# Performance work log

Hardware: AMD Instinct MI355X
Metric: run time of the kernel (lower is better)

Reference implementation:

```python
import jax, jax.numpy as jnp
import numpy as np

B, T, D = 2048, 60, 6
H, F, O = 64, 10, 1


def setup_inputs() -> dict:
    key = jax.random.key(0)
    ks = jax.random.split(key, 16)
    w = lambda k, shape, s=0.1: jax.random.normal(k, shape, jnp.float32) * s
    return {
        "x": jax.random.normal(ks[0], (B, T, D), jnp.float32),
        "W_i": w(ks[1], (D, H)), "U_i": w(ks[2], (H, H)), "b_i": jnp.zeros((H,), jnp.float32),
        "W_ste": w(ks[3], (D, H)), "U_ste": w(ks[4], (H, H)), "b_ste": jnp.ones((H,), jnp.float32),
        "W_fre": w(ks[5], (D, F)), "U_fre": w(ks[6], (H, F)), "b_fre": jnp.ones((F,), jnp.float32),
        "W_c": w(ks[7], (D, H)), "U_c": w(ks[8], (H, H)), "b_c": jnp.zeros((H,), jnp.float32),
        "W_o": w(ks[9], (D, H)), "U_o": w(ks[10], (H, H)), "b_o": jnp.zeros((H,), jnp.float32),
        "U_a": w(ks[11], (F, 1)), "b_a": jnp.zeros((H,), jnp.float32),
        "W_p": w(ks[12], (H, O)), "b_p": jnp.zeros((O,), jnp.float32),
    }


def _hsig(v):
    # torch.nn.Hardsigmoid: relu6(x + 3) / 6
    return jnp.clip(v / 6.0 + 0.5, 0.0, 1.0)


def reference(x, W_i, U_i, b_i, W_ste, U_ste, b_ste, W_fre, U_fre, b_fre,
              W_c, U_c, b_c, W_o, U_o, b_o, U_a, b_a, W_p, b_p):
    b, t_len, _ = x.shape
    h_dim = W_i.shape[1]
    f_dim = W_fre.shape[1]
    freq = jnp.arange(f_dim, dtype=x.dtype) / f_dim  # (F,)
    ua = U_a[:, 0]  # (F,)

    def step(carry, x_t):
        h, S_re, S_im, t = carry
        i = _hsig(x_t @ W_i + b_i + h @ U_i)              # (B,H)
        ste = _hsig(x_t @ W_ste + b_ste + h @ U_ste)      # (B,H)
        fre = _hsig(x_t @ W_fre + b_fre + h @ U_fre)      # (B,F)
        f = ste[:, :, None] * fre[:, None, :]             # (B,H,F)
        c = i * jnp.tanh(x_t @ W_c + b_c + h @ U_c)       # (B,H)
        t = t + 1.0
        omega = (2.0 * jnp.pi) * t * freq                  # (F,)
        S_re = f * S_re + c[:, :, None] * jnp.cos(omega)   # (B,H,F)
        S_im = f * S_im + c[:, :, None] * jnp.sin(omega)   # (B,H,F)
        A = S_re * S_re + S_im * S_im                      # (B,H,F)
        a = jnp.tanh(jnp.einsum('bhf,f->bh', A, ua) + b_a)
        o = _hsig(x_t @ W_o + b_o + h @ U_o)
        h = o * a
        return (h, S_re, S_im, t), None

    init = (jnp.zeros((b, h_dim), x.dtype),
            jnp.zeros((b, h_dim, f_dim), x.dtype),
            jnp.zeros((b, h_dim, f_dim), x.dtype),
            jnp.asarray(0.0, x.dtype))
    (h, _, _, _), _ = jax.lax.scan(step, init, jnp.swapaxes(x, 0, 1))
    # original returns p from the last timestep only
    return h @ W_p + b_p
```

## Files before the change

### kernel.cpp

```cpp
#include <hip/hip_runtime.h>


#define BB 2048
#define TT 60
#define DD 6
#define HH 64
#define FF 10

typedef short bf16x8 __attribute__((ext_vector_type(8)));
typedef float f32x4  __attribute__((ext_vector_type(4)));

__device__ __forceinline__ unsigned short f2bf(float f) {
    union { float f; unsigned u; } v; v.f = f;
    unsigned r = v.u + 0x7fffu + ((v.u >> 16) & 1u);
    return (unsigned short)(r >> 16);
}
__device__ __forceinline__ float bf2f(unsigned short b) {
    union { unsigned u; float f; } v; v.u = ((unsigned)b) << 16; return v.f;
}

__device__ __forceinline__ float hsig_f(float v) {
    return fminf(fmaxf(fmaf(v, 0.16666666666666666f, 0.5f), 0.0f), 1.0f);
}
__device__ __forceinline__ float tanh_f(float x) {
    float xc = fminf(fmaxf(x, -12.0f), 12.0f);
    float e  = __builtin_amdgcn_exp2f(xc * 2.8853900817779268f);
    return (e - 1.0f) * __builtin_amdgcn_rcpf(e + 1.0f);
}
__device__ __forceinline__ float uni(float v) {
    return __int_as_float(__builtin_amdgcn_readfirstlane(__float_as_int(v)));
}
__device__ __forceinline__ void pinv(bf16x8& v) { asm volatile("" : "+v"(v)); }

__global__ __launch_bounds__(256)
__attribute__((amdgpu_waves_per_eu(1, 1)))
void sfm_kernel(
    const float* __restrict__ x,
    const float* __restrict__ W_i,  const float* __restrict__ U_i,  const float* __restrict__ b_i,
    const float* __restrict__ W_ste,const float* __restrict__ U_ste,const float* __restrict__ b_ste,
    const float* __restrict__ W_fre,const float* __restrict__ U_fre,const float* __restrict__ b_fre,
    const float* __restrict__ W_c,  const float* __restrict__ U_c,  const float* __restrict__ b_c,
    const float* __restrict__ W_o,  const float* __restrict__ U_o,  const float* __restrict__ b_o,
    const float* __restrict__ U_a,  const float* __restrict__ b_a,
    const float* __restrict__ W_p,  const float* __restrict__ b_p,
    float* __restrict__ out)
{
    const int tid  = threadIdx.x;
    const int lane = tid & 63;
    const int wave = tid >> 6;
    const int q    = lane >> 4;
    const int n16  = lane & 15;
    const int b0   = blockIdx.x * 8;

    __shared__ __align__(16) float xbuf[8 * TT * DD];
    __shared__ __align__(16) float hbuf[8 * 68];
    __shared__ __align__(16) float zbuf[4 * 64 * 12];
    __shared__ __align__(16) float frebuf[16 * 12];

    {
        const float4* xg = (const float4*)(x + (size_t)b0 * TT * DD);
        float4* xs = (float4*)xbuf;
        for (int i = tid; i < (8 * TT * DD) / 4; i += 256) xs[i] = xg[i];
    }
    for (int i = tid; i < 8 * 68; i += 256) hbuf[i] = 0.0f;

    const float* Ug = (wave == 0) ? U_i : (wave == 1) ? U_ste : (wave == 2) ? U_c : U_o;
    const float* Wg = (wave == 0) ? W_i : (wave == 1) ? W_ste : (wave == 2) ? W_c : W_o;
    const float* bg = (wave == 0) ? b_i : (wave == 1) ? b_ste : (wave == 2) ? b_c : b_o;

    bf16x8 Bh[5][3], Bl[5][3];
    #pragma unroll
    for (int t = 0; t < 5; ++t) {
        #pragma unroll
        for (int c = 0; c < 3; ++c) {
            #pragma unroll
            for (int j = 0; j < 8; ++j) {
                const int kv = c * 32 + q * 8 + j;
                float v = 0.0f;
                if (t < 4) {
                    const int n = t * 16 + n16;
                    if      (kv < 64) v = Ug[kv * HH + n];
                    else if (kv < 70) v = Wg[(kv - 64) * HH + n];
                    else if (kv == 70) v = bg[n];
                } else if (wave == 3 && n16 < FF) {
                    if      (kv < 64) v = U_fre[kv * FF + n16];
                    else if (kv < 70) v = W_fre[(kv - 64) * FF + n16];
                    else if (kv == 70) v = b_fre[n16];
                }
                const unsigned short hb = f2bf(v);
                const float lo = v - bf2f(hb);
                Bh[t][c][j] = (short)hb;
                Bl[t][c][j] = (short)f2bf(lo);
            }
            pinv(Bh[t][c]); pinv(Bl[t][c]);
        }
    }

    const int pb = tid >> 5;
    const int pp = tid & 31;
    const float ba0 = b_a[pp], ba1 = b_a[pp + 32];
    const float wp0 = W_p[pp], wp1 = W_p[pp + 32];
    const float bpv = uni(b_p[0]);
    float uav[FF];
    #pragma unroll
    for (int f = 0; f < FF; ++f) uav[f] = uni(U_a[f]);

    const float CBt[FF] = { 1.0f,  0.8090169943749475f,  0.30901699437494745f,
                           -0.30901699437494745f, -0.8090169943749475f, -1.0f,
                           -0.8090169943749475f, -0.30901699437494745f,
                            0.30901699437494745f,  0.8090169943749475f };
    const float SBt[FF] = { 0.0f,  0.5877852522924731f,  0.9510565162951535f,
                            0.9510565162951535f,  0.5877852522924731f,  0.0f,
                           -0.5877852522924731f, -0.9510565162951535f,
                           -0.9510565162951535f, -0.5877852522924731f };

    float Sre0[FF], Sim0[FF], Sre1[FF], Sim1[FF], cs[FF], sn[FF];
    #pragma unroll
    for (int f = 0; f < FF; ++f) {
        Sre0[f] = 0.0f; Sim0[f] = 0.0f; Sre1[f] = 0.0f; Sim1[f] = 0.0f;
        cs[f] = CBt[f]; sn[f] = SBt[f];
    }
    float h0v = 0.0f, h1v = 0.0f;

    __syncthreads();

    int sm = 0;
    for (int s = 0; s < TT; ++s) {
        bf16x8 Ah[3], Al[3];
        {
            const int ab = n16 & 7;
            #pragma unroll
            for (int c = 0; c < 2; ++c) {
                const float* hp = &hbuf[ab * 68 + c * 32 + q * 8];
                const float4 v0 = *(const float4*)hp;
                const float4 v1 = *(const float4*)(hp + 4);
                const float tv[8] = {v0.x, v0.y, v0.z, v0.w, v1.x, v1.y, v1.z, v1.w};
                #pragma unroll
                for (int j = 0; j < 8; ++j) {
                    const unsigned short hb = f2bf(tv[j]);
                    const float lo = tv[j] - bf2f(hb);
                    Ah[c][j] = (short)hb; Al[c][j] = (short)f2bf(lo);
                }
            }
            float tv[8] = {0, 0, 0, 0, 0, 0, 0, 0};
            if (q == 0) {
                const float2* x2 = (const float2*)&xbuf[ab * (TT * DD) + s * DD];
                const float2 a = x2[0], b = x2[1], c2 = x2[2];
                tv[0] = a.x; tv[1] = a.y; tv[2] = b.x; tv[3] = b.y; tv[4] = c2.x; tv[5] = c2.y;
                tv[6] = 1.0f;
            }
            #pragma unroll
            for (int j = 0; j < 8; ++j) {
                const unsigned short hb = f2bf(tv[j]);
                const float lo = tv[j] - bf2f(hb);
                Ah[2][j] = (short)hb; Al[2][j] = (short)f2bf(lo);
            }
        }

        f32x4 acc[5];
        #pragma unroll
        for (int t = 0; t < 5; ++t) {
            if (t < 4 || wave == 3) {
                f32x4 a = {0.0f, 0.0f, 0.0f, 0.0f};
                #pragma unroll
                for (int c = 0; c < 3; ++c) {
                    a = __builtin_amdgcn_mfma_f32_16x16x32_bf16(Al[c], Bh[t][c], a, 0, 0, 0);
                    a = __builtin_amdgcn_mfma_f32_16x16x32_bf16(Ah[c], Bl[t][c], a, 0, 0, 0);
                    a = __builtin_amdgcn_mfma_f32_16x16x32_bf16(Ah[c], Bh[t][c], a, 0, 0, 0);
                }
                acc[t] = a;
            }
        }

        if (lane < 32) {
            #pragma unroll
            for (int t = 0; t < 4; ++t)
                *(f32x4*)&zbuf[(wave * 64 + t * 16 + n16) * 12 + q * 4] = acc[t];
            if (wave == 3 && n16 < FF)
                *(f32x4*)&frebuf[n16 * 12 + q * 4] = acc[4];
        }
        __syncthreads();

        const float zi0 = zbuf[(0 * 64 + pp) * 12 + pb], zi1 = zbuf[(0 * 64 + pp + 32) * 12 + pb];
        const float zs0 = zbuf[(1 * 64 + pp) * 12 + pb], zs1 = zbuf[(1 * 64 + pp + 32) * 12 + pb];
        const float zc0 = zbuf[(2 * 64 + pp) * 12 + pb], zc1 = zbuf[(2 * 64 + pp + 32) * 12 + pb];
        const float zo0 = zbuf[(3 * 64 + pp) * 12 + pb], zo1 = zbuf[(3 * 64 + pp + 32) * 12 + pb];
        float fr[FF];
        #pragma unroll
        for (int f = 0; f < FF; ++f) fr[f] = hsig_f(frebuf[f * 12 + pb]);

        const float i0 = hsig_f(zi0), st0 = hsig_f(zs0), o0 = hsig_f(zo0);
        const float i1 = hsig_f(zi1), st1 = hsig_f(zs1), o1 = hsig_f(zo1);
        const float c0 = i0 * tanh_f(zc0);
        const float c1 = i1 * tanh_f(zc1);

        if (sm == 0) {
            #pragma unroll
            for (int f = 0; f < FF; ++f) { cs[f] = CBt[f]; sn[f] = SBt[f]; }
        }

        float a0 = ba0, a1 = ba1;
        #pragma unroll
        for (int f = 0; f < FF; ++f) {
            const float fc0 = st0 * fr[f], fc1 = st1 * fr[f];
            Sre0[f] = fmaf(fc0, Sre0[f], c0 * cs[f]);
            Sim0[f] = fmaf(fc0, Sim0[f], c0 * sn[f]);
            Sre1[f] = fmaf(fc1, Sre1[f], c1 * cs[f]);
            Sim1[f] = fmaf(fc1, Sim1[f], c1 * sn[f]);
            const float A0 = fmaf(Sim0[f], Sim0[f], Sre0[f] * Sre0[f]);
            const float A1 = fmaf(Sim1[f], Sim1[f], Sre1[f] * Sre1[f]);
            a0 = fmaf(A0, uav[f], a0);
            a1 = fmaf(A1, uav[f], a1);
            const float cc = cs[f];
            cs[f] = fmaf(cc, CBt[f], -(sn[f] * SBt[f]));
            sn[f] = fmaf(cc, SBt[f],   sn[f] * CBt[f]);
        }
        h0v = o0 * tanh_f(a0);
        h1v = o1 * tanh_f(a1);
        hbuf[pb * 68 + pp]      = h0v;
        hbuf[pb * 68 + pp + 32] = h1v;
        if (++sm == 10) sm = 0;
        __syncthreads();
    }

    float val = fmaf(h0v, wp0, h1v * wp1);
    #pragma unroll
    for (int off = 16; off > 0; off >>= 1) val += __shfl_xor(val, off, 64);
    if (pp == 0) out[b0 + pb] = val + bpv;
}

extern "C" void kernel_launch(void* const* d_in, const int* in_sizes, int n_in,
                              void* d_out, int out_size, void* d_ws, size_t ws_size,
                              hipStream_t stream) {
    (void)in_sizes; (void)n_in; (void)d_ws; (void)ws_size; (void)out_size;
    const float* x     = (const float*)d_in[0];
    const float* W_i   = (const float*)d_in[1];
    const float* U_i   = (const float*)d_in[2];
    const float* b_i   = (const float*)d_in[3];
    const float* W_ste = (const float*)d_in[4];
    const float* U_ste = (const float*)d_in[5];
    const float* b_ste = (const float*)d_in[6];
    const float* W_fre = (const float*)d_in[7];
    const float* U_fre = (const float*)d_in[8];
    const float* b_fre = (const float*)d_in[9];
    const float* W_c   = (const float*)d_in[10];
    const float* U_c   = (const float*)d_in[11];
    const float* b_c   = (const float*)d_in[12];
    const float* W_o   = (const float*)d_in[13];
    const float* U_o   = (const float*)d_in[14];
    const float* b_o   = (const float*)d_in[15];
    const float* U_a   = (const float*)d_in[16];
    const float* b_a   = (const float*)d_in[17];
    const float* W_p   = (const float*)d_in[18];
    const float* b_p   = (const float*)d_in[19];

    sfm_kernel<<<BB / 8, 256, 0, stream>>>(
        x, W_i, U_i, b_i, W_ste, U_ste, b_ste, W_fre, U_fre, b_fre,
        W_c, U_c, b_c, W_o, U_o, b_o, U_a, b_a, W_p, b_p, (float*)d_out);
}
```

Before: 182.0 us.

## Store h and x as pre-split bf16 hi/lo in LDS, remap thread-to-element layout

```diff
diff --git a/kernel.cpp b/kernel.cpp
--- a/kernel.cpp
+++ b/kernel.cpp
@@ -7,6 +7,9 @@
 #define HH 64
 #define FF 10
 
+#define XS 968
+#define HS 72
+
 typedef short bf16x8 __attribute__((ext_vector_type(8)));
 typedef float f32x4  __attribute__((ext_vector_type(4)));
 
@@ -18,7 +21,6 @@
 __device__ __forceinline__ float bf2f(unsigned short b) {
     union { unsigned u; float f; } v; v.u = ((unsigned)b) << 16; return v.f;
 }
-
 __device__ __forceinline__ float hsig_f(float v) {
     return fminf(fmaxf(fmaf(v, 0.16666666666666666f, 0.5f), 0.0f), 1.0f);
 }
@@ -52,17 +54,28 @@
     const int n16  = lane & 15;
     const int b0   = blockIdx.x * 8;
 
-    __shared__ __align__(16) float xbuf[8 * TT * DD];
-    __shared__ __align__(16) float hbuf[8 * 68];
+    __shared__ __align__(16) unsigned short xsp[8 * XS];
+    __shared__ __align__(16) unsigned short hhi[8 * HS];
+    __shared__ __align__(16) unsigned short hlo[8 * HS];
     __shared__ __align__(16) float zbuf[4 * 64 * 12];
     __shared__ __align__(16) float frebuf[16 * 12];
-
-    {
-        const float4* xg = (const float4*)(x + (size_t)b0 * TT * DD);
-        float4* xs = (float4*)xbuf;
-        for (int i = tid; i < (8 * TT * DD) / 4; i += 256) xs[i] = xg[i];
-    }
-    for (int i = tid; i < 8 * 68; i += 256) hbuf[i] = 0.0f;
+    __shared__ float red[4][8];
+
+    for (int item = tid; item < 8 * TT; item += 256) {
+        const float* xg = x + (size_t)b0 * (TT * DD) + item * DD;
+        const int b = item / TT, s = item - b * TT;
+        unsigned short* dst = &xsp[b * XS + s * 16];
+        #pragma unroll
+        for (int d = 0; d < DD; ++d) {
+            const float v = xg[d];
+            const unsigned short hb = f2bf(v);
+            dst[d]     = hb;
+            dst[8 + d] = f2bf(v - bf2f(hb));
+        }
+        dst[6] = 0x3F80; dst[7] = 0;
+        dst[14] = 0; dst[15] = 0;
+    }
+    for (int i = tid; i < 8 * HS; i += 256) { hhi[i] = 0; hlo[i] = 0; }
 
     const float* Ug = (wave == 0) ? U_i : (wave == 1) ? U_ste : (wave == 2) ? U_c : U_o;
     const float* Wg = (wave == 0) ? W_i : (wave == 1) ? W_ste : (wave == 2) ? W_c : W_o;
@@ -79,27 +92,26 @@
                 float v = 0.0f;
                 if (t < 4) {
                     const int n = t * 16 + n16;
-                    if      (kv < 64) v = Ug[kv * HH + n];
-                    else if (kv < 70) v = Wg[(kv - 64) * HH + n];
+                    if      (kv < 64)  v = Ug[kv * HH + n];
+                    else if (kv < 70)  v = Wg[(kv - 64) * HH + n];
                     else if (kv == 70) v = bg[n];
                 } else if (wave == 3 && n16 < FF) {
-                    if      (kv < 64) v = U_fre[kv * FF + n16];
-                    else if (kv < 70) v = W_fre[(kv - 64) * FF + n16];
+                    if      (kv < 64)  v = U_fre[kv * FF + n16];
+                    else if (kv < 70)  v = W_fre[(kv - 64) * FF + n16];
                     else if (kv == 70) v = b_fre[n16];
                 }
                 const unsigned short hb = f2bf(v);
-                const float lo = v - bf2f(hb);
                 Bh[t][c][j] = (short)hb;
-                Bl[t][c][j] = (short)f2bf(lo);
+                Bl[t][c][j] = (short)f2bf(v - bf2f(hb));
             }
             pinv(Bh[t][c]); pinv(Bl[t][c]);
         }
     }
 
-    const int pb = tid >> 5;
-    const int pp = tid & 31;
-    const float ba0 = b_a[pp], ba1 = b_a[pp + 32];
-    const float wp0 = W_p[pp], wp1 = W_p[pp + 32];
+    const int pb = tid & 7;
+    const int pc = tid >> 3;
+    const float ba0 = b_a[pc], ba1 = b_a[pc + 32];
+    const float wp0 = W_p[pc], wp1 = W_p[pc + 32];
     const float bpv = uni(b_p[0]);
     float uav[FF];
     #pragma unroll
@@ -126,35 +138,19 @@
 
     int sm = 0;
     for (int s = 0; s < TT; ++s) {
+        const int ab = n16 & 7;
         bf16x8 Ah[3], Al[3];
+        #pragma unroll
+        for (int c = 0; c < 2; ++c) {
+            Ah[c] = *(const bf16x8*)&hhi[ab * HS + c * 32 + q * 8];
+            Al[c] = *(const bf16x8*)&hlo[ab * HS + c * 32 + q * 8];
+        }
         {
-            const int ab = n16 & 7;
-            #pragma unroll
-            for (int c = 0; c < 2; ++c) {
-                const float* hp = &hbuf[ab * 68 + c * 32 + q * 8];
-                const float4 v0 = *(const float4*)hp;
-                const float4 v1 = *(const float4*)(hp + 4);
-                const float tv[8] = {v0.x, v0.y, v0.z, v0.w, v1.x, v1.y, v1.z, v1.w};
-                #pragma unroll
-                for (int j = 0; j < 8; ++j) {
-                    const unsigned short hb = f2bf(tv[j]);
-                    const float lo = tv[j] - bf2f(hb);
-                    Ah[c][j] = (short)hb; Al[c][j] = (short)f2bf(lo);
-                }
-            }
-            float tv[8] = {0, 0, 0, 0, 0, 0, 0, 0};
-            if (q == 0) {
-                const float2* x2 = (const float2*)&xbuf[ab * (TT * DD) + s * DD];
-                const float2 a = x2[0], b = x2[1], c2 = x2[2];
-                tv[0] = a.x; tv[1] = a.y; tv[2] = b.x; tv[3] = b.y; tv[4] = c2.x; tv[5] = c2.y;
-                tv[6] = 1.0f;
-            }
-            #pragma unroll
-            for (int j = 0; j < 8; ++j) {
-                const unsigned short hb = f2bf(tv[j]);
-                const float lo = tv[j] - bf2f(hb);
-                Ah[2][j] = (short)hb; Al[2][j] = (short)f2bf(lo);
-            }
+            const bf16x8 xvh = *(const bf16x8*)&xsp[ab * XS + s * 16];
+            const bf16x8 xvl = *(const bf16x8*)&xsp[ab * XS + s * 16 + 8];
+            const bf16x8 zf = {0, 0, 0, 0, 0, 0, 0, 0};
+            Ah[2] = (q == 0) ? xvh : zf;
+            Al[2] = (q == 0) ? xvl : zf;
         }
 
         f32x4 acc[5];
@@ -181,10 +177,10 @@
         }
         __syncthreads();
 
-        const float zi0 = zbuf[(0 * 64 + pp) * 12 + pb], zi1 = zbuf[(0 * 64 + pp + 32) * 12 + pb];
-        const float zs0 = zbuf[(1 * 64 + pp) * 12 + pb], zs1 = zbuf[(1 * 64 + pp + 32) * 12 + pb];
-        const float zc0 = zbuf[(2 * 64 + pp) * 12 + pb], zc1 = zbuf[(2 * 64 + pp + 32) * 12 + pb];
-        const float zo0 = zbuf[(3 * 64 + pp) * 12 + pb], zo1 = zbuf[(3 * 64 + pp + 32) * 12 + pb];
+        const float zi0 = zbuf[(0 * 64 + pc) * 12 + pb], zi1 = zbuf[(0 * 64 + pc + 32) * 12 + pb];
+        const float zs0 = zbuf[(1 * 64 + pc) * 12 + pb], zs1 = zbuf[(1 * 64 + pc + 32) * 12 + pb];
+        const float zc0 = zbuf[(2 * 64 + pc) * 12 + pb], zc1 = zbuf[(2 * 64 + pc + 32) * 12 + pb];
+        const float zo0 = zbuf[(3 * 64 + pc) * 12 + pb], zo1 = zbuf[(3 * 64 + pc + 32) * 12 + pb];
         float fr[FF];
         #pragma unroll
         for (int f = 0; f < FF; ++f) fr[f] = hsig_f(frebuf[f * 12 + pb]);
@@ -217,16 +213,27 @@
         }
         h0v = o0 * tanh_f(a0);
         h1v = o1 * tanh_f(a1);
-        hbuf[pb * 68 + pp]      = h0v;
-        hbuf[pb * 68 + pp + 32] = h1v;
+
+        {
+            const unsigned short h0b = f2bf(h0v);
+            const unsigned short h1b = f2bf(h1v);
+            hhi[pb * HS + pc]      = h0b;
+            hhi[pb * HS + pc + 32] = h1b;
+            hlo[pb * HS + pc]      = f2bf(h0v - bf2f(h0b));
+            hlo[pb * HS + pc + 32] = f2bf(h1v - bf2f(h1b));
+        }
         if (++sm == 10) sm = 0;
         __syncthreads();
     }
 
     float val = fmaf(h0v, wp0, h1v * wp1);
-    #pragma unroll
-    for (int off = 16; off > 0; off >>= 1) val += __shfl_xor(val, off, 64);
-    if (pp == 0) out[b0 + pb] = val + bpv;
+    val += __shfl_xor(val, 8, 64);
+    val += __shfl_xor(val, 16, 64);
+    val += __shfl_xor(val, 32, 64);
+    if ((lane >> 3) == 0) red[wave][pb] = val;
+    __syncthreads();
+    if (tid < 8)
+        out[b0 + tid] = red[0][tid] + red[1][tid] + red[2][tid] + red[3][tid] + bpv;
 }
 
 extern "C" void kernel_launch(void* const* d_in, const int* in_sizes, int n_in,
```

Result: faster. 164.4 us (-9.7%).
